# Performance work log

Hardware: AMD Instinct MI355X
Metric: run time of the kernel (lower is better)

The kernel has to match this reference:

```python
import jax, jax.numpy as jnp
import numpy as np

HIDDEN = 2048
NUM_HEAD = 32
GROUP = 8
HEAD_DIM = HIDDEN // NUM_HEAD  # 64
REP = NUM_HEAD // GROUP        # 4


def setup_inputs() -> dict:
    key = jax.random.key(0)
    ks = jax.random.split(key, 9)
    s = 0.02
    kv_dim = GROUP * HEAD_DIM
    return {
        "hidden_states": jax.random.normal(ks[0], (2, 2048, HIDDEN), dtype=jnp.float32),
        "Wq": jax.random.normal(ks[1], (HIDDEN, HIDDEN), dtype=jnp.float32) * s,
        "bq": jnp.zeros((HIDDEN,), dtype=jnp.float32),
        "Wk": jax.random.normal(ks[2], (HIDDEN, kv_dim), dtype=jnp.float32) * s,
        "bk": jnp.zeros((kv_dim,), dtype=jnp.float32),
        "Wv": jax.random.normal(ks[3], (HIDDEN, kv_dim), dtype=jnp.float32) * s,
        "bv": jnp.zeros((kv_dim,), dtype=jnp.float32),
        "Wo": jax.random.normal(ks[4], (HIDDEN, HIDDEN), dtype=jnp.float32) * s,
        "bo": jnp.zeros((HIDDEN,), dtype=jnp.float32),
    }


def reference(hidden_states, Wq, bq, Wk, bk, Wv, bv, Wo, bo):
    B, S, H = hidden_states.shape
    q = hidden_states @ Wq + bq                      # [B,S,H]
    k = hidden_states @ Wk + bk                      # [B,S,G*hd]
    v = hidden_states @ Wv + bv
    q = q.reshape(B, S, NUM_HEAD, HEAD_DIM).transpose(0, 2, 1, 3)   # [B,nh,S,hd]
    k = k.reshape(B, S, GROUP, HEAD_DIM).transpose(0, 2, 1, 3)      # [B,G,S,hd]
    v = v.reshape(B, S, GROUP, HEAD_DIM).transpose(0, 2, 1, 3)
    # expand KV heads: each group head repeated REP times contiguously
    k = jnp.repeat(k, REP, axis=1)                   # [B,nh,S,hd]
    v = jnp.repeat(v, REP, axis=1)
    scale = 1.0 / jnp.sqrt(jnp.float32(HEAD_DIM))
    scores = jnp.einsum("bhqd,bhkd->bhqk", q, k) * scale  # [B,nh,S,S]
    attn = jax.nn.softmax(scores, axis=-1)
    out = jnp.einsum("bhqk,bhkd->bhqd", attn, v)     # [B,nh,S,hd]
    out = out.transpose(0, 2, 1, 3).reshape(B, S, NUM_HEAD * HEAD_DIM)
    return out @ Wo + bo
```

## Files before the change

kernel.cpp:

```cpp
#include <hip/hip_runtime.h>
#include <hip/hip_bf16.h>

typedef __attribute__((ext_vector_type(8))) short bf16x8;
typedef __attribute__((ext_vector_type(4))) short bf16x4;
typedef __attribute__((ext_vector_type(4))) float f32x4;

__device__ __forceinline__ unsigned short f2bf(float f) {
  union { float f; unsigned int u; } v; v.f = f;
  unsigned int r = (v.u + 0x7fffu + ((v.u >> 16) & 1u)) >> 16;
  return (unsigned short)r;
}

__device__ __forceinline__ unsigned int pk2bf(float a, float b) {
  float2 t; t.x = a; t.y = b;
  __hip_bfloat162 h = __float22bfloat162_rn(t);
  union { __hip_bfloat162 h; unsigned int u; } cv; cv.h = h;
  return cv.u;
}

__device__ __forceinline__ void g2l16(unsigned short* lds, const unsigned short* g) {
  __builtin_amdgcn_global_load_lds(
      (const __attribute__((address_space(1))) unsigned int*)g,
      (__attribute__((address_space(3))) unsigned int*)lds, 16, 0, 0);
}


__global__ __launch_bounds__(256) void cast_hs_kernel(const float* __restrict__ in,
                                                      unsigned short* __restrict__ out) {
  size_t i = (size_t)blockIdx.x * 256 + threadIdx.x;
  float4 v = ((const float4*)in)[i];
  ushort4 o;
  o.x = f2bf(v.x); o.y = f2bf(v.y); o.z = f2bf(v.z); o.w = f2bf(v.w);
  ((ushort4*)out)[i] = o;
}

__global__ __launch_bounds__(256) void transpose_all_kernel(
    const float* __restrict__ Wq, const float* __restrict__ Wk,
    const float* __restrict__ Wv, const float* __restrict__ Wo,
    unsigned short* __restrict__ Wqkv, unsigned short* __restrict__ WoT) {
  __shared__ float tile[32][33];
  int z = blockIdx.z;
  const float* src; unsigned short* dst; int N;
  if (z == 0)      { src = Wq; dst = Wqkv;                          N = 2048; }
  else if (z == 1) { src = Wk; dst = Wqkv + (size_t)2048 * 2048;    N = 512; }
  else if (z == 2) { src = Wv; dst = Wqkv + (size_t)2560 * 2048;    N = 512; }
  else             { src = Wo; dst = WoT;                           N = 2048; }
  if (blockIdx.x * 32 >= N) return;
  int n0 = blockIdx.x * 32, k0 = blockIdx.y * 32;
  int t = threadIdx.x;
  for (int i = 0; i < 4; ++i) {
    int linear = i * 256 + t;
    int kr = linear >> 5, nc = linear & 31;
    tile[kr][nc] = src[(size_t)(k0 + kr) * N + (n0 + nc)];
  }
  __syncthreads();
  for (int i = 0; i < 4; ++i) {
    int linear = i * 256 + t;
    int nr = linear >> 5, kc = linear & 31;
    dst[(size_t)(n0 + nr) * 2048 + (k0 + kc)] = f2bf(tile[kc][nr]);
  }
}


#define QSCALE 0.18033688011112042f

__global__ __launch_bounds__(256) void gemm_qkv_kernel(
    const unsigned short* __restrict__ A, const unsigned short* __restrict__ Bt,
    const float* __restrict__ bq, const float* __restrict__ bk, const float* __restrict__ bv,
    unsigned short* __restrict__ Qb, unsigned short* __restrict__ Kb,
    unsigned short* __restrict__ Vtb) {
  __shared__ __align__(16) unsigned short smem[128 * 136];
  unsigned short* sA = smem;
  unsigned short* sB = smem + 4096;
  const int K = 2048;
  int bm0 = blockIdx.y * 128, bn0 = blockIdx.x * 128;
  int t = threadIdx.x;
  int w = t >> 6, lane = t & 63, l16 = lane & 15, quad = lane >> 4;
  int wm = (w & 1) * 64, wn = (w >> 1) * 64;
  f32x4 zero = {0.f, 0.f, 0.f, 0.f};
  f32x4 acc[4][4];
  for (int mt = 0; mt < 4; ++mt)
    for (int nt = 0; nt < 4; ++nt) acc[mt][nt] = zero;

  for (int k0 = 0; k0 < K; k0 += 32) {
    for (int i = 0; i < 2; ++i) {
      int linear = i * 256 + t;
      int row = linear >> 2, kofs = (linear & 3) * 8;
      g2l16(sA + linear * 8, A + (size_t)(bm0 + row) * K + k0 + kofs);
      g2l16(sB + linear * 8, Bt + (size_t)(bn0 + row) * K + k0 + kofs);
    }
    __syncthreads();
    bf16x8 af[4], bfr[4];
    for (int mt = 0; mt < 4; ++mt)
      af[mt] = *(const bf16x8*)(sA + (wm + mt * 16 + l16) * 32 + quad * 8);
    for (int nt = 0; nt < 4; ++nt)
      bfr[nt] = *(const bf16x8*)(sB + (wn + nt * 16 + l16) * 32 + quad * 8);
    for (int mt = 0; mt < 4; ++mt)
      for (int nt = 0; nt < 4; ++nt)
        acc[mt][nt] = __builtin_amdgcn_mfma_f32_16x16x32_bf16(af[mt], bfr[nt], acc[mt][nt], 0, 0, 0);
    __syncthreads();
  }

  const int SP = 136;
  bool isV = (bn0 >= 2560);
  bool isQ = (bn0 < 2048);
  const float* bias = isQ ? bq : (bn0 < 2560 ? bk : bv);
  int nbase = isQ ? 0 : (bn0 < 2560 ? 2048 : 2560);

  for (int nt = 0; nt < 4; ++nt) {
    int nl = wn + nt * 16 + l16;
    float bb = bias[bn0 + nl - nbase];
    for (int mt = 0; mt < 4; ++mt)
      for (int r = 0; r < 4; ++r) {
        int ml = wm + mt * 16 + quad * 4 + r;
        float fv = acc[mt][nt][r] + bb;
        if (isQ) fv *= QSCALE;
        unsigned short val = f2bf(fv);
        if (isV) smem[nl * SP + ml] = val;
        else     smem[ml * SP + nl] = val;
      }
  }
  __syncthreads();

  int b = bm0 >> 11, s0 = bm0 & 2047;
  if (bn0 < 2048) {
    for (int i = 0; i < 8; ++i) {
      int idx = i * 256 + t;
      int sub = idx >> 10, s_l = (idx >> 3) & 127, dch = (idx & 7) * 8;
      bf16x8 v = *(const bf16x8*)(smem + s_l * SP + sub * 64 + dch);
      int n = bn0 + sub * 64 + dch;
      int h = n >> 6, d = n & 63;
      *(bf16x8*)(Qb + (((size_t)b * 32 + h) * 2048 + s0 + s_l) * 64 + d) = v;
    }
  } else if (bn0 < 2560) {
    for (int i = 0; i < 8; ++i) {
      int idx = i * 256 + t;
      int sub = idx >> 10, s_l = (idx >> 3) & 127, dch = (idx & 7) * 8;
      bf16x8 v = *(const bf16x8*)(smem + s_l * SP + sub * 64 + dch);
      int nn = bn0 + sub * 64 + dch - 2048;
      int g = nn >> 6, d = nn & 63;
      *(bf16x8*)(Kb + (((size_t)b * 8 + g) * 2048 + s0 + s_l) * 64 + d) = v;
    }
  } else {
    for (int i = 0; i < 8; ++i) {
      int idx = i * 256 + t;
      int nl = idx >> 4, sj = (idx & 15) * 8;
      bf16x8 v = *(const bf16x8*)(smem + nl * SP + sj);
      int nn = bn0 + nl - 2560;
      int g = nn >> 6, d = nn & 63;
      *(bf16x8*)(Vtb + (((size_t)b * 8 + g) * 64 + d) * 2048 + s0 + sj) = v;
    }
  }
}


__global__ __launch_bounds__(512, 4) void attn_kernel(
    const unsigned short* __restrict__ Qb, const unsigned short* __restrict__ Kb,
    const unsigned short* __restrict__ Vtb, unsigned short* __restrict__ AttnB) {
  __shared__ __align__(16) unsigned short Kt[2 * 4096];
  __shared__ __align__(16) unsigned short Vt[2 * 4096];
  int qt = blockIdx.x, h = blockIdx.y, b = blockIdx.z;
  int g = h >> 2;
  int t = threadIdx.x, w = t >> 6, lane = t & 63, l16 = lane & 15, quad = lane >> 4;

  const unsigned short* qb0 =
      Qb + (((size_t)b * 32 + h) * 2048 + qt * 256 + w * 16 + l16) * 64 + quad * 8;
  const unsigned short* qb1 = qb0 + (size_t)128 * 64;
  bf16x8 aQ0a = *(const bf16x8*)(qb0);
  bf16x8 aQ1a = *(const bf16x8*)(qb0 + 32);
  bf16x8 aQ0b = *(const bf16x8*)(qb1);
  bf16x8 aQ1b = *(const bf16x8*)(qb1 + 32);

  const unsigned short* kbase = Kb + ((size_t)b * 8 + g) * (2048 * 64);
  const unsigned short* vbase = Vtb + ((size_t)b * 8 + g) * (64 * 2048);
  int r_ = t & 63, c_ = t >> 6;
  const unsigned short* gK = kbase + (size_t)r_ * 64 + c_ * 8;
  const unsigned short* gV = vbase + (size_t)r_ * 2048 + c_ * 8;

  auto stage = [&](int buf, int kb) {
    g2l16(Kt + buf * 4096 + t * 8, gK + (size_t)kb * 4096);
    g2l16(Vt + buf * 4096 + t * 8, gV + (size_t)kb * 64);
  };

  f32x4 zero = {0.f, 0.f, 0.f, 0.f};
  f32x4 m10 = {-10.f, -10.f, -10.f, -10.f};
  union { unsigned short s[4]; bf16x4 v; } ones;
  ones.s[0] = 0x3F80; ones.s[1] = 0x3F80; ones.s[2] = 0x3F80; ones.s[3] = 0x3F80;

  f32x4 oA[4], oB[4], olA, olB;
  for (int dt = 0; dt < 4; ++dt) { oA[dt] = zero; oB[dt] = zero; }
  olA = zero; olB = zero;

  stage(0, 0);
  __syncthreads();
  int cur = 0;
  for (int kb = 0; kb < 32; ++kb) {
    if (kb < 31) stage(cur ^ 1, kb + 1);
    const unsigned short* Kc = Kt + cur * 4096;
    const unsigned short* Vc = Vt + cur * 4096;

    for (int nt = 0; nt < 4; ++nt) {
      bf16x8 bk0 = *(const bf16x8*)(Kc + (quad * 64 + nt * 16 + l16) * 8);
      bf16x8 bk1 = *(const bf16x8*)(Kc + ((quad + 4) * 64 + nt * 16 + l16) * 8);
      f32x4 stA = __builtin_amdgcn_mfma_f32_16x16x32_bf16(bk0, aQ0a, m10, 0, 0, 0);
      stA = __builtin_amdgcn_mfma_f32_16x16x32_bf16(bk1, aQ1a, stA, 0, 0, 0);
      f32x4 stB = __builtin_amdgcn_mfma_f32_16x16x32_bf16(bk0, aQ0b, m10, 0, 0, 0);
      stB = __builtin_amdgcn_mfma_f32_16x16x32_bf16(bk1, aQ1b, stB, 0, 0, 0);

      union { unsigned int u[2]; bf16x4 v; } paA, paB;
      paA.u[0] = pk2bf(__builtin_amdgcn_exp2f(stA[0]), __builtin_amdgcn_exp2f(stA[1]));
      paA.u[1] = pk2bf(__builtin_amdgcn_exp2f(stA[2]), __builtin_amdgcn_exp2f(stA[3]));
      paB.u[0] = pk2bf(__builtin_amdgcn_exp2f(stB[0]), __builtin_amdgcn_exp2f(stB[1]));
      paB.u[1] = pk2bf(__builtin_amdgcn_exp2f(stB[2]), __builtin_amdgcn_exp2f(stB[3]));

      olA = __builtin_amdgcn_mfma_f32_16x16x16bf16_1k(paA.v, ones.v, olA, 0, 0, 0);
      olB = __builtin_amdgcn_mfma_f32_16x16x16bf16_1k(paB.v, ones.v, olB, 0, 0, 0);

      int c = nt * 2 + (quad >> 1);
      int ho = (quad & 1) * 4;
      for (int dt = 0; dt < 4; ++dt) {
        bf16x4 bv = *(const bf16x4*)(Vc + (c * 64 + dt * 16 + l16) * 8 + ho);
        oA[dt] = __builtin_amdgcn_mfma_f32_16x16x16bf16_1k(paA.v, bv, oA[dt], 0, 0, 0);
        oB[dt] = __builtin_amdgcn_mfma_f32_16x16x16bf16_1k(paB.v, bv, oB[dt], 0, 0, 0);
      }
    }
    __syncthreads();
    cur ^= 1;
  }

  for (int r = 0; r < 4; ++r) {
    float invA = 1.f / olA[r];
    float invB = 1.f / olB[r];
    int srow0 = qt * 256 + w * 16 + quad * 4 + r;
    size_t base0 = ((size_t)b * 2048 + srow0) * 2048 + h * 64;
    size_t base1 = base0 + (size_t)128 * 2048;
    for (int dt = 0; dt < 4; ++dt) {
      AttnB[base0 + dt * 16 + l16] = f2bf(oA[dt][r] * invA);
      AttnB[base1 + dt * 16 + l16] = f2bf(oB[dt][r] * invB);
    }
  }
}


__global__ __launch_bounds__(256) void gemm_out_kernel(
    const unsigned short* __restrict__ A, const unsigned short* __restrict__ Bt,
    const float* __restrict__ bo, float* __restrict__ out) {
  __shared__ __align__(16) unsigned short sA[128 * 32];
  __shared__ __align__(16) unsigned short sB[128 * 32];
  const int K = 2048;
  int bm0 = blockIdx.y * 128, bn0 = blockIdx.x * 128;
  int t = threadIdx.x;
  int w = t >> 6, lane = t & 63, l16 = lane & 15, quad = lane >> 4;
  int wm = (w & 1) * 64, wn = (w >> 1) * 64;
  f32x4 zero = {0.f, 0.f, 0.f, 0.f};
  f32x4 acc[4][4];
  for (int mt = 0; mt < 4; ++mt)
    for (int nt = 0; nt < 4; ++nt) acc[mt][nt] = zero;

  for (int k0 = 0; k0 < K; k0 += 32) {
    for (int i = 0; i < 2; ++i) {
      int linear = i * 256 + t;
      int row = linear >> 2, kofs = (linear & 3) * 8;
      g2l16(sA + linear * 8, A + (size_t)(bm0 + row) * K + k0 + kofs);
      g2l16(sB + linear * 8, Bt + (size_t)(bn0 + row) * K + k0 + kofs);
    }
    __syncthreads();
    bf16x8 af[4], bfr[4];
    for (int mt = 0; mt < 4; ++mt)
      af[mt] = *(const bf16x8*)(sA + (wm + mt * 16 + l16) * 32 + quad * 8);
    for (int nt = 0; nt < 4; ++nt)
      bfr[nt] = *(const bf16x8*)(sB + (wn + nt * 16 + l16) * 32 + quad * 8);
    for (int mt = 0; mt < 4; ++mt)
      for (int nt = 0; nt < 4; ++nt)
        acc[mt][nt] = __builtin_amdgcn_mfma_f32_16x16x32_bf16(af[mt], bfr[nt], acc[mt][nt], 0, 0, 0);
    __syncthreads();
  }

  for (int nt = 0; nt < 4; ++nt) {
    int n = bn0 + wn + nt * 16 + l16;
    float bias = bo[n];
    for (int mt = 0; mt < 4; ++mt)
      for (int r = 0; r < 4; ++r) {
        int m = bm0 + wm + mt * 16 + quad * 4 + r;
        out[(size_t)m * 2048 + n] = acc[mt][nt][r] + bias;
      }
  }
}


extern "C" void kernel_launch(void* const* d_in, const int* in_sizes, int n_in,
                              void* d_out, int out_size, void* d_ws, size_t ws_size,
                              hipStream_t stream) {
  const float* hs = (const float*)d_in[0];
  const float* Wq = (const float*)d_in[1];
  const float* bq = (const float*)d_in[2];
  const float* Wk = (const float*)d_in[3];
  const float* bk = (const float*)d_in[4];
  const float* Wv = (const float*)d_in[5];
  const float* bv = (const float*)d_in[6];
  const float* Wo = (const float*)d_in[7];
  const float* bo = (const float*)d_in[8];
  float* out = (float*)d_out;

  char* ws = (char*)d_ws;
  unsigned short* hsb   = (unsigned short*)(ws);
  unsigned short* Wqkv  = (unsigned short*)(ws + 16777216);
  unsigned short* WoT   = (unsigned short*)(ws + 29360128);
  unsigned short* Qb    = (unsigned short*)(ws + 37748736);
  unsigned short* Kb    = (unsigned short*)(ws + 54525952);
  unsigned short* Vtb   = (unsigned short*)(ws + 58720256);
  unsigned short* AttnB = (unsigned short*)(ws + 62914560);

  hipLaunchKernelGGL(cast_hs_kernel, dim3(8192), dim3(256), 0, stream, hs, hsb);
  hipLaunchKernelGGL(transpose_all_kernel, dim3(64, 64, 4), dim3(256), 0, stream,
                     Wq, Wk, Wv, Wo, Wqkv, WoT);
  hipLaunchKernelGGL(gemm_qkv_kernel, dim3(24, 32), dim3(256), 0, stream,
                     hsb, Wqkv, bq, bk, bv, Qb, Kb, Vtb);
  hipLaunchKernelGGL(attn_kernel, dim3(8, 32, 2), dim3(512), 0, stream, Qb, Kb, Vtb, AttnB);
  hipLaunchKernelGGL(gemm_out_kernel, dim3(16, 32), dim3(256), 0, stream, AttnB, WoT, bo, out);
}
```

Before: 312.5 us.

## Double-buffer GEMM K-loop with BK=64, XOR-swizzled LDS and async prefetch

Both the QKV projection GEMM and the output projection GEMM now share a new K-loop helper. It widens the K tile from 32 to 64 and double-buffers LDS so the global-to-LDS loads for the next tile overlap the MFMA work on the current one. It XOR-swizzles the 16-byte chunks in LDS to cut bank conflicts on fragment reads, and raises wave priority around the MFMA block. LDS use grows to 64 KB per block, which may limit occupancy, and correctness depends on the hand-written vmcnt waits and barriers.

```diff
diff --git a/kernel.cpp b/kernel.cpp
--- a/kernel.cpp
+++ b/kernel.cpp
@@ -62,6 +62,66 @@
 }
 
 
+__device__ __forceinline__ void kloop_bk64(
+    const unsigned short* __restrict__ A, const unsigned short* __restrict__ Bt,
+    unsigned short* sA, unsigned short* sB,
+    int bm0, int bn0, int t, f32x4 acc[4][4]) {
+  const int K = 2048;
+  int w = t >> 6, lane = t & 63, l16 = lane & 15, quad = lane >> 4;
+  int wm = (w & 1) * 64, wn = (w >> 1) * 64;
+
+  auto stage = [&](int buf, int k0) {
+    for (int i = 0; i < 4; ++i) {
+      int linear = i * 256 + t;
+      int row = linear >> 3, ch = linear & 7;
+      int kofs = (ch ^ (row & 7)) * 8;
+      g2l16(sA + buf * 8192 + linear * 8, A + (size_t)(bm0 + row) * K + k0 + kofs);
+      g2l16(sB + buf * 8192 + linear * 8, Bt + (size_t)(bn0 + row) * K + k0 + kofs);
+    }
+  };
+
+  stage(0, 0);
+  stage(1, 64);
+  asm volatile("s_waitcnt vmcnt(8)" ::: "memory");
+  __builtin_amdgcn_s_barrier();
+  __builtin_amdgcn_sched_barrier(0);
+
+  int cur = 0;
+  for (int k0 = 0; k0 < K; k0 += 64) {
+    const unsigned short* cA = sA + cur * 8192;
+    const unsigned short* cB = sB + cur * 8192;
+#pragma unroll
+    for (int kk = 0; kk < 2; ++kk) {
+      bf16x8 af[4], bfr[4];
+      for (int mt = 0; mt < 4; ++mt) {
+        int r = wm + mt * 16 + l16;
+        af[mt] = *(const bf16x8*)(cA + r * 64 + ((kk * 4 + quad) ^ (r & 7)) * 8);
+      }
+      for (int nt = 0; nt < 4; ++nt) {
+        int r = wn + nt * 16 + l16;
+        bfr[nt] = *(const bf16x8*)(cB + r * 64 + ((kk * 4 + quad) ^ (r & 7)) * 8);
+      }
+      __builtin_amdgcn_s_setprio(1);
+      for (int mt = 0; mt < 4; ++mt)
+        for (int nt = 0; nt < 4; ++nt)
+          acc[mt][nt] = __builtin_amdgcn_mfma_f32_16x16x32_bf16(af[mt], bfr[nt], acc[mt][nt], 0, 0, 0);
+      __builtin_amdgcn_s_setprio(0);
+    }
+    __builtin_amdgcn_s_barrier();
+    __builtin_amdgcn_sched_barrier(0);
+    if (k0 + 128 < K) {
+      stage(cur, k0 + 128);
+      asm volatile("s_waitcnt vmcnt(8)" ::: "memory");
+    } else {
+      asm volatile("s_waitcnt vmcnt(0)" ::: "memory");
+    }
+    __builtin_amdgcn_s_barrier();
+    __builtin_amdgcn_sched_barrier(0);
+    cur ^= 1;
+  }
+}
+
+
 #define QSCALE 0.18033688011112042f
 
 __global__ __launch_bounds__(256) void gemm_qkv_kernel(
@@ -69,10 +129,10 @@
     const float* __restrict__ bq, const float* __restrict__ bk, const float* __restrict__ bv,
     unsigned short* __restrict__ Qb, unsigned short* __restrict__ Kb,
     unsigned short* __restrict__ Vtb) {
-  __shared__ __align__(16) unsigned short smem[128 * 136];
-  unsigned short* sA = smem;
-  unsigned short* sB = smem + 4096;
-  const int K = 2048;
+  __shared__ __align__(16) unsigned short lds[4 * 8192];
+  unsigned short* sA = lds;
+  unsigned short* sB = lds + 16384;
+  unsigned short* smem = lds;
   int bm0 = blockIdx.y * 128, bn0 = blockIdx.x * 128;
   int t = threadIdx.x;
   int w = t >> 6, lane = t & 63, l16 = lane & 15, quad = lane >> 4;
@@ -82,24 +142,8 @@
   for (int mt = 0; mt < 4; ++mt)
     for (int nt = 0; nt < 4; ++nt) acc[mt][nt] = zero;
 
-  for (int k0 = 0; k0 < K; k0 += 32) {
-    for (int i = 0; i < 2; ++i) {
-      int linear = i * 256 + t;
-      int row = linear >> 2, kofs = (linear & 3) * 8;
-      g2l16(sA + linear * 8, A + (size_t)(bm0 + row) * K + k0 + kofs);
-      g2l16(sB + linear * 8, Bt + (size_t)(bn0 + row) * K + k0 + kofs);
-    }
-    __syncthreads();
-    bf16x8 af[4], bfr[4];
-    for (int mt = 0; mt < 4; ++mt)
-      af[mt] = *(const bf16x8*)(sA + (wm + mt * 16 + l16) * 32 + quad * 8);
-    for (int nt = 0; nt < 4; ++nt)
-      bfr[nt] = *(const bf16x8*)(sB + (wn + nt * 16 + l16) * 32 + quad * 8);
-    for (int mt = 0; mt < 4; ++mt)
-      for (int nt = 0; nt < 4; ++nt)
-        acc[mt][nt] = __builtin_amdgcn_mfma_f32_16x16x32_bf16(af[mt], bfr[nt], acc[mt][nt], 0, 0, 0);
-    __syncthreads();
-  }
+  kloop_bk64(A, Bt, sA, sB, bm0, bn0, t, acc);
+  __syncthreads();
 
   const int SP = 136;
   bool isV = (bn0 >= 2560);
@@ -245,9 +289,9 @@
 __global__ __launch_bounds__(256) void gemm_out_kernel(
     const unsigned short* __restrict__ A, const unsigned short* __restrict__ Bt,
     const float* __restrict__ bo, float* __restrict__ out) {
-  __shared__ __align__(16) unsigned short sA[128 * 32];
-  __shared__ __align__(16) unsigned short sB[128 * 32];
-  const int K = 2048;
+  __shared__ __align__(16) unsigned short lds[4 * 8192];
+  unsigned short* sA = lds;
+  unsigned short* sB = lds + 16384;
   int bm0 = blockIdx.y * 128, bn0 = blockIdx.x * 128;
   int t = threadIdx.x;
   int w = t >> 6, lane = t & 63, l16 = lane & 15, quad = lane >> 4;
@@ -257,24 +301,7 @@
   for (int mt = 0; mt < 4; ++mt)
     for (int nt = 0; nt < 4; ++nt) acc[mt][nt] = zero;
 
-  for (int k0 = 0; k0 < K; k0 += 32) {
-    for (int i = 0; i < 2; ++i) {
-      int linear = i * 256 + t;
-      int row = linear >> 2, kofs = (linear & 3) * 8;
-      g2l16(sA + linear * 8, A + (size_t)(bm0 + row) * K + k0 + kofs);
-      g2l16(sB + linear * 8, Bt + (size_t)(bn0 + row) * K + k0 + kofs);
-    }
-    __syncthreads();
-    bf16x8 af[4], bfr[4];
-    for (int mt = 0; mt < 4; ++mt)
-      af[mt] = *(const bf16x8*)(sA + (wm + mt * 16 + l16) * 32 + quad * 8);
-    for (int nt = 0; nt < 4; ++nt)
-      bfr[nt] = *(const bf16x8*)(sB + (wn + nt * 16 + l16) * 32 + quad * 8);
-    for (int mt = 0; mt < 4; ++mt)
-      for (int nt = 0; nt < 4; ++nt)
-        acc[mt][nt] = __builtin_amdgcn_mfma_f32_16x16x32_bf16(af[mt], bfr[nt], acc[mt][nt], 0, 0, 0);
-    __syncthreads();
-  }
+  kloop_bk64(A, Bt, sA, sB, bm0, bn0, t, acc);
 
   for (int nt = 0; nt < 4; ++nt) {
     int n = bn0 + wn + nt * 16 + l16;
```

Result: no change. 313.0 us (+0.2%).

## Rewrite QKV GEMM as 256x256 tile, double-buffered, swizzled LDS pipeline

Applied to the files above, without the earlier changes.

The QKV projection GEMM goes from 128x128 tiles with 256 threads and a single-buffered, fully synchronised K loop to 256x256 tiles with 512 threads. The K step grows to 64, and global-to-LDS loads are double-buffered and interleaved with MFMA phases. LDS rows use an XOR swizzle to avoid bank conflicts, and MFMA issue priority is raised around the compute. The aim is to hide load latency and increase data reuse per tile, at the cost of 128KB of LDS per block and only 192 blocks, which may underfill the GPU.

```diff
diff --git a/kernel.cpp b/kernel.cpp
--- a/kernel.cpp
+++ b/kernel.cpp
@@ -64,91 +64,159 @@
 
 #define QSCALE 0.18033688011112042f
 
-__global__ __launch_bounds__(256) void gemm_qkv_kernel(
+#define QKV_PHASE(BUFO, MH, KK, SSTAGE, STA, DOSTAGE, GATE)                          \
+  do {                                                                               \
+    __builtin_amdgcn_sched_barrier(0);                                               \
+    bf16x8 af[4], bfr[4];                                                            \
+    _Pragma("unroll")                                                                \
+    for (int m4 = 0; m4 < 4; ++m4) {                                                 \
+      int lr = ((MH) * 4 + m4) * 16 + l16;                                           \
+      af[m4] = *(const bf16x8*)(sA + (BUFO) + wm * 8192 + lr * 64 +                  \
+                                ((((KK) * 4 + quad) ^ (lr & 7)) * 8));               \
+    }                                                                                \
+    _Pragma("unroll")                                                                \
+    for (int nr = 0; nr < 4; ++nr) {                                                 \
+      int cb = wn * 64 + nr * 16;                                                    \
+      int lc = (cb & 127) + l16;                                                     \
+      bfr[nr] = *(const bf16x8*)(sB + (BUFO) + (cb >> 7) * 8192 + lc * 64 +          \
+                                 ((((KK) * 4 + quad) ^ (lc & 7)) * 8));              \
+    }                                                                                \
+    if (DOSTAGE) {                                                                   \
+      const unsigned short* src_ = (STA) ? A : Bt;                                   \
+      unsigned short* dst_ = (STA) ? sA : sB;                                        \
+      int b0_ = (STA) ? bm0 : bn0;                                                   \
+      int dbase_ = ((SSTAGE) & 1) * 16384;                                           \
+      _Pragma("unroll")                                                              \
+      for (int h_ = 0; h_ < 2; ++h_)                                                 \
+        _Pragma("unroll")                                                            \
+        for (int ii_ = 0; ii_ < 2; ++ii_) {                                          \
+          int lin_ = ii_ * 512 + t;                                                  \
+          int row_ = lin_ >> 3, ch_ = lin_ & 7;                                      \
+          g2l16(dst_ + dbase_ + h_ * 8192 + lin_ * 8,                                \
+                src_ + (size_t)(b0_ + h_ * 128 + row_) * 2048 + (SSTAGE) * 64 +      \
+                    ((ch_ ^ (row_ & 7)) * 8));                                       \
+        }                                                                            \
+    }                                                                                \
+    if (GATE) asm volatile("s_waitcnt vmcnt(0)" ::: "memory");                       \
+    __builtin_amdgcn_s_barrier();                                                    \
+    asm volatile("s_waitcnt lgkmcnt(0)" ::: "memory");                               \
+    __builtin_amdgcn_sched_barrier(0);                                               \
+    __builtin_amdgcn_s_setprio(1);                                                   \
+    _Pragma("unroll")                                                                \
+    for (int m4 = 0; m4 < 4; ++m4)                                                   \
+      _Pragma("unroll")                                                              \
+      for (int nr = 0; nr < 4; ++nr)                                                 \
+        acc[(MH) * 4 + m4][nr] = __builtin_amdgcn_mfma_f32_16x16x32_bf16(            \
+            af[m4], bfr[nr], acc[(MH) * 4 + m4][nr], 0, 0, 0);                       \
+    __builtin_amdgcn_s_setprio(0);                                                   \
+  } while (0)
+
+__global__ __launch_bounds__(512, 2) void gemm_qkv_kernel(
     const unsigned short* __restrict__ A, const unsigned short* __restrict__ Bt,
     const float* __restrict__ bq, const float* __restrict__ bk, const float* __restrict__ bv,
     unsigned short* __restrict__ Qb, unsigned short* __restrict__ Kb,
     unsigned short* __restrict__ Vtb) {
-  __shared__ __align__(16) unsigned short smem[128 * 136];
-  unsigned short* sA = smem;
-  unsigned short* sB = smem + 4096;
-  const int K = 2048;
-  int bm0 = blockIdx.y * 128, bn0 = blockIdx.x * 128;
+  __shared__ __align__(16) unsigned short lds[65536];
+  unsigned short* sA = lds;
+  unsigned short* sB = lds + 32768;
+  int bm0 = blockIdx.y * 256, bn0 = blockIdx.x * 256;
   int t = threadIdx.x;
-  int w = t >> 6, lane = t & 63, l16 = lane & 15, quad = lane >> 4;
-  int wm = (w & 1) * 64, wn = (w >> 1) * 64;
+  int lane = t & 63, l16 = lane & 15, quad = lane >> 4;
+  int w = t >> 6, wm = w >> 2, wn = w & 3;
+
   f32x4 zero = {0.f, 0.f, 0.f, 0.f};
-  f32x4 acc[4][4];
-  for (int mt = 0; mt < 4; ++mt)
-    for (int nt = 0; nt < 4; ++nt) acc[mt][nt] = zero;
-
-  for (int k0 = 0; k0 < K; k0 += 32) {
-    for (int i = 0; i < 2; ++i) {
-      int linear = i * 256 + t;
-      int row = linear >> 2, kofs = (linear & 3) * 8;
-      g2l16(sA + linear * 8, A + (size_t)(bm0 + row) * K + k0 + kofs);
-      g2l16(sB + linear * 8, Bt + (size_t)(bn0 + row) * K + k0 + kofs);
-    }
-    __syncthreads();
-    bf16x8 af[4], bfr[4];
-    for (int mt = 0; mt < 4; ++mt)
-      af[mt] = *(const bf16x8*)(sA + (wm + mt * 16 + l16) * 32 + quad * 8);
-    for (int nt = 0; nt < 4; ++nt)
-      bfr[nt] = *(const bf16x8*)(sB + (wn + nt * 16 + l16) * 32 + quad * 8);
-    for (int mt = 0; mt < 4; ++mt)
-      for (int nt = 0; nt < 4; ++nt)
-        acc[mt][nt] = __builtin_amdgcn_mfma_f32_16x16x32_bf16(af[mt], bfr[nt], acc[mt][nt], 0, 0, 0);
-    __syncthreads();
-  }
-
+  f32x4 acc[8][4];
+#pragma unroll
+  for (int m = 0; m < 8; ++m)
+#pragma unroll
+    for (int n = 0; n < 4; ++n) acc[m][n] = zero;
+
+#pragma unroll
+  for (int h = 0; h < 2; ++h)
+#pragma unroll
+    for (int ii = 0; ii < 2; ++ii) {
+      int lin = ii * 512 + t;
+      int row = lin >> 3, ch = lin & 7;
+      int kofs = (ch ^ (row & 7)) * 8;
+      g2l16(sA + h * 8192 + lin * 8, A + (size_t)(bm0 + h * 128 + row) * 2048 + kofs);
+      g2l16(sB + h * 8192 + lin * 8, Bt + (size_t)(bn0 + h * 128 + row) * 2048 + kofs);
+    }
+  asm volatile("s_waitcnt vmcnt(0)" ::: "memory");
+  __builtin_amdgcn_s_barrier();
+
+  for (int i = 0; i < 16; ++i) {
+    int s1 = 2 * i + 1, s2 = 2 * i + 2;
+    QKV_PHASE(0,     0, 0, s1, 1, 1, 0);
+    QKV_PHASE(0,     0, 1, s1, 0, 1, 0);
+    QKV_PHASE(0,     1, 0, 0,  0, 0, 0);
+    QKV_PHASE(0,     1, 1, 0,  0, 0, 1);
+    QKV_PHASE(16384, 0, 0, s2, 1, 1, 0);
+    QKV_PHASE(16384, 0, 1, s2, 0, 1, 0);
+    QKV_PHASE(16384, 1, 0, 0,  0, 0, 0);
+    QKV_PHASE(16384, 1, 1, 0,  0, 0, 1);
+  }
+  asm volatile("s_waitcnt vmcnt(0) lgkmcnt(0)" ::: "memory");
+  __syncthreads();
+
+  unsigned short* smem = lds;
   const int SP = 136;
   bool isV = (bn0 >= 2560);
   bool isQ = (bn0 < 2048);
   const float* bias = isQ ? bq : (bn0 < 2560 ? bk : bv);
   int nbase = isQ ? 0 : (bn0 < 2560 ? 2048 : 2560);
 
-  for (int nt = 0; nt < 4; ++nt) {
-    int nl = wn + nt * 16 + l16;
-    float bb = bias[bn0 + nl - nbase];
-    for (int mt = 0; mt < 4; ++mt)
-      for (int r = 0; r < 4; ++r) {
-        int ml = wm + mt * 16 + quad * 4 + r;
-        float fv = acc[mt][nt][r] + bb;
-        if (isQ) fv *= QSCALE;
-        unsigned short val = f2bf(fv);
-        if (isV) smem[nl * SP + ml] = val;
-        else     smem[ml * SP + nl] = val;
+  for (int qm = 0; qm < 2; ++qm) {
+    for (int qn = 0; qn < 2; ++qn) {
+      int bm0q = bm0 + qm * 128, bn0q = bn0 + qn * 128;
+      if (wm == qm && (wn >> 1) == qn) {
+#pragma unroll
+        for (int nrep = 0; nrep < 4; ++nrep) {
+          int nl = (wn & 1) * 64 + nrep * 16 + l16;
+          float bb = bias[bn0q + nl - nbase];
+#pragma unroll
+          for (int mrep = 0; mrep < 8; ++mrep)
+#pragma unroll
+            for (int r = 0; r < 4; ++r) {
+              int ml = mrep * 16 + quad * 4 + r;
+              float fv = acc[mrep][nrep][r] + bb;
+              if (isQ) fv *= QSCALE;
+              unsigned short val = f2bf(fv);
+              if (isV) smem[nl * SP + ml] = val;
+              else     smem[ml * SP + nl] = val;
+            }
+        }
       }
-  }
-  __syncthreads();
-
-  int b = bm0 >> 11, s0 = bm0 & 2047;
-  if (bn0 < 2048) {
-    for (int i = 0; i < 8; ++i) {
-      int idx = i * 256 + t;
-      int sub = idx >> 10, s_l = (idx >> 3) & 127, dch = (idx & 7) * 8;
-      bf16x8 v = *(const bf16x8*)(smem + s_l * SP + sub * 64 + dch);
-      int n = bn0 + sub * 64 + dch;
-      int h = n >> 6, d = n & 63;
-      *(bf16x8*)(Qb + (((size_t)b * 32 + h) * 2048 + s0 + s_l) * 64 + d) = v;
-    }
-  } else if (bn0 < 2560) {
-    for (int i = 0; i < 8; ++i) {
-      int idx = i * 256 + t;
-      int sub = idx >> 10, s_l = (idx >> 3) & 127, dch = (idx & 7) * 8;
-      bf16x8 v = *(const bf16x8*)(smem + s_l * SP + sub * 64 + dch);
-      int nn = bn0 + sub * 64 + dch - 2048;
-      int g = nn >> 6, d = nn & 63;
-      *(bf16x8*)(Kb + (((size_t)b * 8 + g) * 2048 + s0 + s_l) * 64 + d) = v;
-    }
-  } else {
-    for (int i = 0; i < 8; ++i) {
-      int idx = i * 256 + t;
-      int nl = idx >> 4, sj = (idx & 15) * 8;
-      bf16x8 v = *(const bf16x8*)(smem + nl * SP + sj);
-      int nn = bn0 + nl - 2560;
-      int g = nn >> 6, d = nn & 63;
-      *(bf16x8*)(Vtb + (((size_t)b * 8 + g) * 64 + d) * 2048 + s0 + sj) = v;
+      __syncthreads();
+      int b = bm0q >> 11, s0 = bm0q & 2047;
+      if (isQ) {
+        for (int i2 = 0; i2 < 4; ++i2) {
+          int idx = i2 * 512 + t;
+          int sub = idx >> 10, s_l = (idx >> 3) & 127, dch = (idx & 7) * 8;
+          bf16x8 v = *(const bf16x8*)(smem + s_l * SP + sub * 64 + dch);
+          int n = bn0q + sub * 64 + dch;
+          int h = n >> 6, d = n & 63;
+          *(bf16x8*)(Qb + (((size_t)b * 32 + h) * 2048 + s0 + s_l) * 64 + d) = v;
+        }
+      } else if (!isV) {
+        for (int i2 = 0; i2 < 4; ++i2) {
+          int idx = i2 * 512 + t;
+          int sub = idx >> 10, s_l = (idx >> 3) & 127, dch = (idx & 7) * 8;
+          bf16x8 v = *(const bf16x8*)(smem + s_l * SP + sub * 64 + dch);
+          int nn = bn0q + sub * 64 + dch - 2048;
+          int g = nn >> 6, d = nn & 63;
+          *(bf16x8*)(Kb + (((size_t)b * 8 + g) * 2048 + s0 + s_l) * 64 + d) = v;
+        }
+      } else {
+        for (int i2 = 0; i2 < 4; ++i2) {
+          int idx = i2 * 512 + t;
+          int nl = idx >> 4, sj = (idx & 15) * 8;
+          bf16x8 v = *(const bf16x8*)(smem + nl * SP + sj);
+          int nn = bn0q + nl - 2560;
+          int g = nn >> 6, d = nn & 63;
+          *(bf16x8*)(Vtb + (((size_t)b * 8 + g) * 64 + d) * 2048 + s0 + sj) = v;
+        }
+      }
+      __syncthreads();
     }
   }
 }
@@ -314,7 +382,7 @@
   hipLaunchKernelGGL(cast_hs_kernel, dim3(8192), dim3(256), 0, stream, hs, hsb);
   hipLaunchKernelGGL(transpose_all_kernel, dim3(64, 64, 4), dim3(256), 0, stream,
                      Wq, Wk, Wv, Wo, Wqkv, WoT);
-  hipLaunchKernelGGL(gemm_qkv_kernel, dim3(24, 32), dim3(256), 0, stream,
+  hipLaunchKernelGGL(gemm_qkv_kernel, dim3(12, 16), dim3(512), 0, stream,
                      hsb, Wqkv, bq, bk, bv, Qb, Kb, Vtb);
   hipLaunchKernelGGL(attn_kernel, dim3(8, 32, 2), dim3(512), 0, stream, Qb, Kb, Vtb, AttnB);
   hipLaunchKernelGGL(gemm_out_kernel, dim3(16, 32), dim3(256), 0, stream, AttnB, WoT, bo, out);
```

Result: slower. 321.4 us (+2.8%).

## Split-K output GEMM with atomics and merge prep kernels with bias init

Applied to the files above, without the earlier changes.

Merges the hidden-state cast and weight transposes into one prep kernel, which also pre-fills the output with the bias. The output projection GEMM is split along K into two halves, doubling the block count, and partial sums are added to the output with float atomics. This aims to improve occupancy and wave count for the final GEMM and to remove one launch. The cost is extra atomic traffic, an added full-output write pass for the bias, and non-deterministic summation order.

```diff
diff --git a/kernel.cpp b/kernel.cpp
--- a/kernel.cpp
+++ b/kernel.cpp
@@ -25,29 +25,40 @@
 }
 
 
-__global__ __launch_bounds__(256) void cast_hs_kernel(const float* __restrict__ in,
-                                                      unsigned short* __restrict__ out) {
-  size_t i = (size_t)blockIdx.x * 256 + threadIdx.x;
-  float4 v = ((const float4*)in)[i];
-  ushort4 o;
-  o.x = f2bf(v.x); o.y = f2bf(v.y); o.z = f2bf(v.z); o.w = f2bf(v.w);
-  ((ushort4*)out)[i] = o;
-}
-
-__global__ __launch_bounds__(256) void transpose_all_kernel(
+__global__ __launch_bounds__(256) void prep_kernel(
+    const float* __restrict__ hs, unsigned short* __restrict__ hsb,
     const float* __restrict__ Wq, const float* __restrict__ Wk,
     const float* __restrict__ Wv, const float* __restrict__ Wo,
-    unsigned short* __restrict__ Wqkv, unsigned short* __restrict__ WoT) {
+    unsigned short* __restrict__ Wqkv, unsigned short* __restrict__ WoT,
+    const float* __restrict__ bo, float* __restrict__ out) {
   __shared__ float tile[32][33];
-  int z = blockIdx.z;
+  int flat = blockIdx.x;
+  int t = threadIdx.x;
+
+  if (flat < 8192) {
+    size_t i = (size_t)flat * 256 + t;
+    float4 v = ((const float4*)hs)[i];
+    ushort4 o;
+    o.x = f2bf(v.x); o.y = f2bf(v.y); o.z = f2bf(v.z); o.w = f2bf(v.w);
+    ((ushort4*)hsb)[i] = o;
+    return;
+  }
+  if (flat >= 24576) {
+    size_t fi = (size_t)(flat - 24576) * 256 + t;
+    float4 b4 = ((const float4*)bo)[fi & 511];
+    ((float4*)out)[fi] = b4;
+    return;
+  }
+  int tb = flat - 8192;
+  int z = tb >> 12, rem = tb & 4095;
+  int bx = rem & 63, by = rem >> 6;
   const float* src; unsigned short* dst; int N;
   if (z == 0)      { src = Wq; dst = Wqkv;                          N = 2048; }
   else if (z == 1) { src = Wk; dst = Wqkv + (size_t)2048 * 2048;    N = 512; }
   else if (z == 2) { src = Wv; dst = Wqkv + (size_t)2560 * 2048;    N = 512; }
   else             { src = Wo; dst = WoT;                           N = 2048; }
-  if (blockIdx.x * 32 >= N) return;
-  int n0 = blockIdx.x * 32, k0 = blockIdx.y * 32;
-  int t = threadIdx.x;
+  if (bx * 32 >= N) return;
+  int n0 = bx * 32, k0 = by * 32;
   for (int i = 0; i < 4; ++i) {
     int linear = i * 256 + t;
     int kr = linear >> 5, nc = linear & 31;
@@ -244,11 +255,12 @@
 
 __global__ __launch_bounds__(256) void gemm_out_kernel(
     const unsigned short* __restrict__ A, const unsigned short* __restrict__ Bt,
-    const float* __restrict__ bo, float* __restrict__ out) {
+    float* __restrict__ out) {
   __shared__ __align__(16) unsigned short sA[128 * 32];
   __shared__ __align__(16) unsigned short sB[128 * 32];
   const int K = 2048;
   int bm0 = blockIdx.y * 128, bn0 = blockIdx.x * 128;
+  int kz = blockIdx.z;
   int t = threadIdx.x;
   int w = t >> 6, lane = t & 63, l16 = lane & 15, quad = lane >> 4;
   int wm = (w & 1) * 64, wn = (w >> 1) * 64;
@@ -257,7 +269,8 @@
   for (int mt = 0; mt < 4; ++mt)
     for (int nt = 0; nt < 4; ++nt) acc[mt][nt] = zero;
 
-  for (int k0 = 0; k0 < K; k0 += 32) {
+  int kbeg = kz * 1024, kend = kbeg + 1024;
+  for (int k0 = kbeg; k0 < kend; k0 += 32) {
     for (int i = 0; i < 2; ++i) {
       int linear = i * 256 + t;
       int row = linear >> 2, kofs = (linear & 3) * 8;
@@ -278,11 +291,10 @@
 
   for (int nt = 0; nt < 4; ++nt) {
     int n = bn0 + wn + nt * 16 + l16;
-    float bias = bo[n];
     for (int mt = 0; mt < 4; ++mt)
       for (int r = 0; r < 4; ++r) {
         int m = bm0 + wm + mt * 16 + quad * 4 + r;
-        out[(size_t)m * 2048 + n] = acc[mt][nt][r] + bias;
+        atomicAdd(&out[(size_t)m * 2048 + n], acc[mt][nt][r]);
       }
   }
 }
@@ -311,11 +323,10 @@
   unsigned short* Vtb   = (unsigned short*)(ws + 58720256);
   unsigned short* AttnB = (unsigned short*)(ws + 62914560);
 
-  hipLaunchKernelGGL(cast_hs_kernel, dim3(8192), dim3(256), 0, stream, hs, hsb);
-  hipLaunchKernelGGL(transpose_all_kernel, dim3(64, 64, 4), dim3(256), 0, stream,
-                     Wq, Wk, Wv, Wo, Wqkv, WoT);
+  hipLaunchKernelGGL(prep_kernel, dim3(32768), dim3(256), 0, stream,
+                     hs, hsb, Wq, Wk, Wv, Wo, Wqkv, WoT, bo, out);
   hipLaunchKernelGGL(gemm_qkv_kernel, dim3(24, 32), dim3(256), 0, stream,
                      hsb, Wqkv, bq, bk, bv, Qb, Kb, Vtb);
   hipLaunchKernelGGL(attn_kernel, dim3(8, 32, 2), dim3(512), 0, stream, Qb, Kb, Vtb, AttnB);
-  hipLaunchKernelGGL(gemm_out_kernel, dim3(16, 32), dim3(256), 0, stream, AttnB, WoT, bo, out);
-}
+  hipLaunchKernelGGL(gemm_out_kernel, dim3(16, 32, 2), dim3(256), 0, stream, AttnB, WoT, out);
+}
```

Result: slower. 359.5 us (+15.0%).
